# Kernel optimization log

Measured on AMD Instinct MI355X. Metric: run time of the kernel, lower is better.

Reference implementation:

```python
import jax, jax.numpy as jnp
import numpy as np

B, N, IN_DIM, HID = 16, 1024, 2, 64
GDEP = 2
ALPHA = 3.0                      # DGCRM/DGCN tanh alpha
GC_ALPHA, GC_BETA, GC_GAMMA = 0.05, 0.95, 0.95  # list_weight
HYPER, MID, NODE_DIM = 32, 16, 40
CIN = HID + IN_DIM               # 66
CAT = (GDEP + 1) * CIN           # 198


def setup_inputs() -> dict:
    key = jax.random.key(0)
    ks = jax.random.split(key, 14)
    x = jax.random.normal(ks[0], (B, N, IN_DIM), jnp.float32)
    hidden_state = 0.1 * jax.random.normal(ks[1], (B, N, HID), jnp.float32)
    nodevec1 = jax.random.normal(ks[2], (N, NODE_DIM), jnp.float32)
    nodevec2 = jax.random.normal(ks[3], (N, NODE_DIM), jnp.float32)
    A0 = jax.random.uniform(ks[4], (N, N), jnp.float32)
    A0 = A0 / A0.sum(-1, keepdims=True)
    A1 = jax.random.uniform(ks[5], (N, N), jnp.float32)
    A1 = A1 / A1.sum(-1, keepdims=True)
    s = 0.05  # small init scale
    hyper_W1 = s * jax.random.normal(ks[6], (4, CAT, HYPER), jnp.float32)
    hyper_b1 = jnp.zeros((4, HYPER), jnp.float32)
    hyper_W2 = s * jax.random.normal(ks[7], (4, HYPER, MID), jnp.float32)
    hyper_b2 = jnp.zeros((4, MID), jnp.float32)
    hyper_W3 = s * jax.random.normal(ks[8], (4, MID, NODE_DIM), jnp.float32)
    hyper_b3 = jnp.zeros((4, NODE_DIM), jnp.float32)
    rnn_W = s * jax.random.normal(ks[9], (6, CAT, HID), jnp.float32)
    rnn_b = jnp.zeros((6, HID), jnp.float32)
    return dict(x=x, hidden_state=hidden_state, nodevec1=nodevec1, nodevec2=nodevec2,
                A0=A0, A1=A1, hyper_W1=hyper_W1, hyper_b1=hyper_b1,
                hyper_W2=hyper_W2, hyper_b2=hyper_b2, hyper_W3=hyper_W3,
                hyper_b3=hyper_b3, rnn_W=rnn_W, rnn_b=rnn_b)


def reference(x, hidden_state, nodevec1, nodevec2, A0, A1,
              hyper_W1, hyper_b1, hyper_W2, hyper_b2, hyper_W3, hyper_b3,
              rnn_W, rnn_b):
    def gconv_hyper(inp, adj, i):
        # K-hop diffusion: h = alpha*x + gamma * (h^T adj) over node dim
        h = inp
        outs = [h]
        for _ in range(GDEP):
            h = GC_ALPHA * inp + GC_GAMMA * jnp.einsum('bnc,nm->bmc', h, adj)
            outs.append(h)
        ho = jnp.concatenate(outs, axis=-1)           # [B,N,(gdep+1)*CIN]
        ho = jax.nn.sigmoid(ho @ hyper_W1[i] + hyper_b1[i])
        ho = jax.nn.sigmoid(ho @ hyper_W2[i] + hyper_b2[i])
        return ho @ hyper_W3[i] + hyper_b3[i]         # [B,N,NODE_DIM]

    def gconv_rnn(inp, i):
        # FAITHFUL to source bug: stray leading '+' makes the beta/gamma
        # einsum terms standalone no-op statements, so each hop is h=alpha*x.
        outs = [inp] + [GC_ALPHA * inp] * GDEP
        return jnp.concatenate(outs, axis=-1) @ rnn_W[i] + rnn_b[i]

    # --- DGCN: dynamic adjacency generation ---
    hyper_input = jnp.concatenate((x, hidden_state), axis=-1)  # [B,N,CIN]
    filter1 = gconv_hyper(hyper_input, A0, 0) + gconv_hyper(hyper_input, A1, 1)
    filter2 = gconv_hyper(hyper_input, A0, 2) + gconv_hyper(hyper_input, A1, 3)
    nv1 = jnp.tanh(ALPHA * nodevec1[None] * filter1)  # [B,N,NODE_DIM]
    nv2 = jnp.tanh(ALPHA * nodevec2[None] * filter2)
    a = jnp.einsum('bnd,bmd->bnm', nv1, nv2) - jnp.einsum('bnd,bmd->bnm', nv2, nv1)
    adp_raw = jax.nn.relu(jnp.tanh(ALPHA * a))        # [B,N,N]
    eye = jnp.eye(N, dtype=adp_raw.dtype)
    def norm(adj):
        adj = adj + eye
        return adj / adj.sum(-1, keepdims=True)
    adp = norm(adp_raw)                               # computed as in source
    adpT = norm(jnp.swapaxes(adp_raw, 1, 2))          # (unused downstream due to
    del adp, adpT                                     #  the GConv_RNN source bug)

    # --- GRU-style gating ---
    combined = jnp.concatenate((x, hidden_state), axis=-1)
    z = jax.nn.sigmoid(gconv_rnn(combined, 0) + gconv_rnn(combined, 1))
    r = jax.nn.sigmoid(gconv_rnn(combined, 2) + gconv_rnn(combined, 3))
    candidate = jnp.concatenate((x, r * hidden_state), axis=-1)
    hc = jnp.tanh(gconv_rnn(candidate, 4) + gconv_rnn(candidate, 5))
    h = z * hidden_state + (1.0 - z) * hc             # [B,N,HID]
    return h
```

## Files before the change

### kernel.cpp

```cpp
#include <hip/hip_runtime.h>
#include <math.h>

#define NTOK   16384
#define CIN_   66
#define HID_   64
#define NCH    192
#define TPB    16

__device__ __forceinline__ float fast_sigmoid(float a) {
    return 1.0f / (1.0f + __expf(-a));
}
__device__ __forceinline__ float fast_tanh(float a) {
    return 1.0f - 2.0f / (__expf(2.0f * a) + 1.0f);
}

__global__ void fold_weights(const float* __restrict__ rnn_W,
                             const float* __restrict__ rnn_b,
                             float* __restrict__ Wf,
                             float* __restrict__ bf)
{
    int idx = blockIdx.x * blockDim.x + threadIdx.x;
    if (idx >= CIN_ * NCH) return;
    int k = idx / NCH;
    int c = idx - k * NCH;
    int g = c >> 6;
    int j = c & 63;
    int i0 = 2 * g, i1 = 2 * g + 1;
    const float s = 0.05f;
    float v = 0.0f;
    v += rnn_W[(i0 * 198 + k) * 64 + j]
       + s * (rnn_W[(i0 * 198 + 66 + k) * 64 + j] + rnn_W[(i0 * 198 + 132 + k) * 64 + j]);
    v += rnn_W[(i1 * 198 + k) * 64 + j]
       + s * (rnn_W[(i1 * 198 + 66 + k) * 64 + j] + rnn_W[(i1 * 198 + 132 + k) * 64 + j]);
    Wf[k * NCH + c] = v;
    if (k == 0) bf[c] = rnn_b[i0 * 64 + j] + rnn_b[i1 * 64 + j];
}

__global__ __launch_bounds__(256)
void dgcrm_gru(const float* __restrict__ x,
               const float* __restrict__ h,
               const float* __restrict__ Wf,
               const float* __restrict__ bf,
               float* __restrict__ out)
{
    __shared__ float C[CIN_][TPB + 1];
    __shared__ float D[CIN_][TPB + 1];
    __shared__ float Z[HID_][TPB + 1];

    const int tid = threadIdx.x;
    const int t0  = blockIdx.x * TPB;

    {
        float4 v = ((const float4*)(h + (size_t)t0 * HID_))[tid];
        int f = tid * 4;
        int t = f >> 6;
        int c = f & 63;
        C[2 + c + 0][t] = v.x;
        C[2 + c + 1][t] = v.y;
        C[2 + c + 2][t] = v.z;
        C[2 + c + 3][t] = v.w;
    }
    if (tid < 2 * TPB) {
        int t = tid >> 1, k = tid & 1;
        float v = x[(size_t)(t0 + t) * 2 + k];
        C[k][t] = v;
        D[k][t] = v;
    }
    __syncthreads();

    const int grp = tid >> 4;
    const int tok = tid & 15;

    {
        const int ch0 = grp * 8;
        float acc[8];
        {
            float4 b0 = *(const float4*)(bf + ch0);
            float4 b1 = *(const float4*)(bf + ch0 + 4);
            acc[0] = b0.x; acc[1] = b0.y; acc[2] = b0.z; acc[3] = b0.w;
            acc[4] = b1.x; acc[5] = b1.y; acc[6] = b1.z; acc[7] = b1.w;
        }
        for (int k = 0; k < CIN_; ++k) {
            float ck = C[k][tok];
            const float4* w4 = (const float4*)(Wf + k * NCH + ch0);
            float4 w0 = w4[0];
            float4 w1 = w4[1];
            acc[0] = fmaf(ck, w0.x, acc[0]);
            acc[1] = fmaf(ck, w0.y, acc[1]);
            acc[2] = fmaf(ck, w0.z, acc[2]);
            acc[3] = fmaf(ck, w0.w, acc[3]);
            acc[4] = fmaf(ck, w1.x, acc[4]);
            acc[5] = fmaf(ck, w1.y, acc[5]);
            acc[6] = fmaf(ck, w1.z, acc[6]);
            acc[7] = fmaf(ck, w1.w, acc[7]);
        }
        if (grp < 8) {
            #pragma unroll
            for (int j = 0; j < 8; ++j)
                Z[ch0 + j][tok] = fast_sigmoid(acc[j]);
        } else {
            const int rb = ch0 - 64;
            #pragma unroll
            for (int j = 0; j < 8; ++j)
                D[2 + rb + j][tok] = fast_sigmoid(acc[j]) * C[2 + rb + j][tok];
        }
    }
    __syncthreads();

    {
        const int c0 = 128 + grp * 4;
        float acc[4];
        {
            float4 b0 = *(const float4*)(bf + c0);
            acc[0] = b0.x; acc[1] = b0.y; acc[2] = b0.z; acc[3] = b0.w;
        }
        for (int k = 0; k < CIN_; ++k) {
            float dk = D[k][tok];
            float4 w = *(const float4*)(Wf + k * NCH + c0);
            acc[0] = fmaf(dk, w.x, acc[0]);
            acc[1] = fmaf(dk, w.y, acc[1]);
            acc[2] = fmaf(dk, w.z, acc[2]);
            acc[3] = fmaf(dk, w.w, acc[3]);
        }
        const int hb = grp * 4;
        #pragma unroll
        for (int j = 0; j < 4; ++j) {
            float hc = fast_tanh(acc[j]);
            float zv = Z[hb + j][tok];
            float hv = C[2 + hb + j][tok];
            Z[hb + j][tok] = zv * hv + (1.0f - zv) * hc;
        }
    }
    __syncthreads();

    {
        int f = tid * 4;
        int t = f >> 6;
        int c = f & 63;
        float4 r;
        r.x = Z[c + 0][t];
        r.y = Z[c + 1][t];
        r.z = Z[c + 2][t];
        r.w = Z[c + 3][t];
        ((float4*)(out + (size_t)t0 * HID_))[tid] = r;
    }
}

extern "C" void kernel_launch(void* const* d_in, const int* in_sizes, int n_in,
                              void* d_out, int out_size, void* d_ws, size_t ws_size,
                              hipStream_t stream)
{
    const float* x     = (const float*)d_in[0];
    const float* hprev = (const float*)d_in[1];
    const float* rnn_W = (const float*)d_in[12];
    const float* rnn_b = (const float*)d_in[13];

    float* Wf = (float*)d_ws;
    float* bf = Wf + CIN_ * NCH;

    fold_weights<<<(CIN_ * NCH + 255) / 256, 256, 0, stream>>>(rnn_W, rnn_b, Wf, bf);
    dgcrm_gru<<<NTOK / TPB, 256, 0, stream>>>(x, hprev, Wf, bf, (float*)d_out);
}
```

Baseline: 110.2 us.

## Process two tokens per thread to reuse weight loads across tokens

Doubles tokens per block from 16 to 32, and each thread now accumulates two tokens against the same loaded weight vectors in both GEMM phases. The aim is to halve global/L1 weight traffic per FMA and raise arithmetic intensity. In exchange it doubles accumulator registers and shared memory per block and halves the number of blocks.

```diff
diff --git a/kernel.cpp b/kernel.cpp
--- a/kernel.cpp
+++ b/kernel.cpp
@@ -5,7 +5,7 @@
 #define CIN_   66
 #define HID_   64
 #define NCH    192
-#define TPB    16
+#define TPB    32
 
 __device__ __forceinline__ float fast_sigmoid(float a) {
     return 1.0f / (1.0f + __expf(-a));
@@ -51,14 +51,19 @@
     const int t0  = blockIdx.x * TPB;
 
     {
-        float4 v = ((const float4*)(h + (size_t)t0 * HID_))[tid];
-        int f = tid * 4;
-        int t = f >> 6;
-        int c = f & 63;
-        C[2 + c + 0][t] = v.x;
-        C[2 + c + 1][t] = v.y;
-        C[2 + c + 2][t] = v.z;
-        C[2 + c + 3][t] = v.w;
+        const float4* h4 = (const float4*)(h + (size_t)t0 * HID_);
+        #pragma unroll
+        for (int r = 0; r < 2; ++r) {
+            int i = tid + r * 256;
+            float4 v = h4[i];
+            int f = i * 4;
+            int t = f >> 6;
+            int c = f & 63;
+            C[2 + c + 0][t] = v.x;
+            C[2 + c + 1][t] = v.y;
+            C[2 + c + 2][t] = v.z;
+            C[2 + c + 3][t] = v.w;
+        }
     }
     if (tid < 2 * TPB) {
         int t = tid >> 1, k = tid & 1;
@@ -68,81 +73,101 @@
     }
     __syncthreads();
 
-    const int grp = tid >> 4;
-    const int tok = tid & 15;
+    const int grp  = tid >> 4;
+    const int tokA = tid & 15;
+    const int tokB = tokA + 16;
 
     {
         const int ch0 = grp * 8;
-        float acc[8];
+        float accA[8], accB[8];
         {
             float4 b0 = *(const float4*)(bf + ch0);
             float4 b1 = *(const float4*)(bf + ch0 + 4);
-            acc[0] = b0.x; acc[1] = b0.y; acc[2] = b0.z; acc[3] = b0.w;
-            acc[4] = b1.x; acc[5] = b1.y; acc[6] = b1.z; acc[7] = b1.w;
+            accA[0] = b0.x; accA[1] = b0.y; accA[2] = b0.z; accA[3] = b0.w;
+            accA[4] = b1.x; accA[5] = b1.y; accA[6] = b1.z; accA[7] = b1.w;
+            #pragma unroll
+            for (int j = 0; j < 8; ++j) accB[j] = accA[j];
         }
         for (int k = 0; k < CIN_; ++k) {
-            float ck = C[k][tok];
+            float ckA = C[k][tokA];
+            float ckB = C[k][tokB];
             const float4* w4 = (const float4*)(Wf + k * NCH + ch0);
             float4 w0 = w4[0];
             float4 w1 = w4[1];
-            acc[0] = fmaf(ck, w0.x, acc[0]);
-            acc[1] = fmaf(ck, w0.y, acc[1]);
-            acc[2] = fmaf(ck, w0.z, acc[2]);
-            acc[3] = fmaf(ck, w0.w, acc[3]);
-            acc[4] = fmaf(ck, w1.x, acc[4]);
-            acc[5] = fmaf(ck, w1.y, acc[5]);
-            acc[6] = fmaf(ck, w1.z, acc[6]);
-            acc[7] = fmaf(ck, w1.w, acc[7]);
+            accA[0] = fmaf(ckA, w0.x, accA[0]);  accB[0] = fmaf(ckB, w0.x, accB[0]);
+            accA[1] = fmaf(ckA, w0.y, accA[1]);  accB[1] = fmaf(ckB, w0.y, accB[1]);
+            accA[2] = fmaf(ckA, w0.z, accA[2]);  accB[2] = fmaf(ckB, w0.z, accB[2]);
+            accA[3] = fmaf(ckA, w0.w, accA[3]);  accB[3] = fmaf(ckB, w0.w, accB[3]);
+            accA[4] = fmaf(ckA, w1.x, accA[4]);  accB[4] = fmaf(ckB, w1.x, accB[4]);
+            accA[5] = fmaf(ckA, w1.y, accA[5]);  accB[5] = fmaf(ckB, w1.y, accB[5]);
+            accA[6] = fmaf(ckA, w1.z, accA[6]);  accB[6] = fmaf(ckB, w1.z, accB[6]);
+            accA[7] = fmaf(ckA, w1.w, accA[7]);  accB[7] = fmaf(ckB, w1.w, accB[7]);
         }
         if (grp < 8) {
             #pragma unroll
-            for (int j = 0; j < 8; ++j)
-                Z[ch0 + j][tok] = fast_sigmoid(acc[j]);
+            for (int j = 0; j < 8; ++j) {
+                Z[ch0 + j][tokA] = fast_sigmoid(accA[j]);
+                Z[ch0 + j][tokB] = fast_sigmoid(accB[j]);
+            }
         } else {
             const int rb = ch0 - 64;
             #pragma unroll
-            for (int j = 0; j < 8; ++j)
-                D[2 + rb + j][tok] = fast_sigmoid(acc[j]) * C[2 + rb + j][tok];
+            for (int j = 0; j < 8; ++j) {
+                D[2 + rb + j][tokA] = fast_sigmoid(accA[j]) * C[2 + rb + j][tokA];
+                D[2 + rb + j][tokB] = fast_sigmoid(accB[j]) * C[2 + rb + j][tokB];
+            }
         }
     }
     __syncthreads();
 
     {
         const int c0 = 128 + grp * 4;
-        float acc[4];
+        float accA[4], accB[4];
         {
             float4 b0 = *(const float4*)(bf + c0);
-            acc[0] = b0.x; acc[1] = b0.y; acc[2] = b0.z; acc[3] = b0.w;
+            accA[0] = b0.x; accA[1] = b0.y; accA[2] = b0.z; accA[3] = b0.w;
+            #pragma unroll
+            for (int j = 0; j < 4; ++j) accB[j] = accA[j];
         }
         for (int k = 0; k < CIN_; ++k) {
-            float dk = D[k][tok];
+            float dkA = D[k][tokA];
+            float dkB = D[k][tokB];
             float4 w = *(const float4*)(Wf + k * NCH + c0);
-            acc[0] = fmaf(dk, w.x, acc[0]);
-            acc[1] = fmaf(dk, w.y, acc[1]);
-            acc[2] = fmaf(dk, w.z, acc[2]);
-            acc[3] = fmaf(dk, w.w, acc[3]);
+            accA[0] = fmaf(dkA, w.x, accA[0]);  accB[0] = fmaf(dkB, w.x, accB[0]);
+            accA[1] = fmaf(dkA, w.y, accA[1]);  accB[1] = fmaf(dkB, w.y, accB[1]);
+            accA[2] = fmaf(dkA, w.z, accA[2]);  accB[2] = fmaf(dkB, w.z, accB[2]);
+            accA[3] = fmaf(dkA, w.w, accA[3]);  accB[3] = fmaf(dkB, w.w, accB[3]);
         }
         const int hb = grp * 4;
         #pragma unroll
         for (int j = 0; j < 4; ++j) {
-            float hc = fast_tanh(acc[j]);
-            float zv = Z[hb + j][tok];
-            float hv = C[2 + hb + j][tok];
-            Z[hb + j][tok] = zv * hv + (1.0f - zv) * hc;
+            float hcA = fast_tanh(accA[j]);
+            float hcB = fast_tanh(accB[j]);
+            float zvA = Z[hb + j][tokA];
+            float zvB = Z[hb + j][tokB];
+            float hvA = C[2 + hb + j][tokA];
+            float hvB = C[2 + hb + j][tokB];
+            Z[hb + j][tokA] = zvA * hvA + (1.0f - zvA) * hcA;
+            Z[hb + j][tokB] = zvB * hvB + (1.0f - zvB) * hcB;
         }
     }
     __syncthreads();
 
     {
-        int f = tid * 4;
-        int t = f >> 6;
-        int c = f & 63;
-        float4 r;
-        r.x = Z[c + 0][t];
-        r.y = Z[c + 1][t];
-        r.z = Z[c + 2][t];
-        r.w = Z[c + 3][t];
-        ((float4*)(out + (size_t)t0 * HID_))[tid] = r;
+        float4* o4 = (float4*)(out + (size_t)t0 * HID_);
+        #pragma unroll
+        for (int r = 0; r < 2; ++r) {
+            int i = tid + r * 256;
+            int f = i * 4;
+            int t = f >> 6;
+            int c = f & 63;
+            float4 v;
+            v.x = Z[c + 0][t];
+            v.y = Z[c + 1][t];
+            v.z = Z[c + 2][t];
+            v.w = Z[c + 3][t];
+            o4[i] = v;
+        }
     }
 }
 
```

After: 102.3 us. 7.1% less time.
